# Optimization experiments

Measured on AMD Instinct MI355X. Metric: run time of the kernel, lower is better.

The kernel has to match this reference:

```python
import jax, jax.numpy as jnp
import numpy as np

N, D, H, C = 50000, 128, 4, 16  # nodes, in_dim, heads, out per head
E, ED = 800000, 64              # edges, edge feature dim
NEG_SLOPE = 0.2


def setup_inputs() -> dict:
    key = jax.random.key(0)
    ks = jax.random.split(key, 10)
    x = jax.random.normal(ks[0], (N, D), dtype=jnp.float32)
    edge_index = jax.random.randint(ks[1], (2, E), 0, N, dtype=jnp.int64)
    edge_attr = jax.random.normal(ks[2], (E, ED), dtype=jnp.float32)
    s = 0.1
    W = jax.random.normal(ks[3], (H * C, D), dtype=jnp.float32) * s       # lin (no bias)
    W_edge = jax.random.normal(ks[4], (H * C, ED), dtype=jnp.float32) * s  # lin_edge (no bias)
    att_src = jax.random.normal(ks[5], (H, C), dtype=jnp.float32) * s
    att_dst = jax.random.normal(ks[6], (H, C), dtype=jnp.float32) * s
    att_edge = jax.random.normal(ks[7], (H, C), dtype=jnp.float32) * s
    bias = jnp.zeros((H * C,), dtype=jnp.float32)
    return dict(x=x, edge_index=edge_index, edge_attr=edge_attr, W=W,
                W_edge=W_edge, att_src=att_src, att_dst=att_dst,
                att_edge=att_edge, bias=bias)


def reference(x, edge_index, edge_attr, W, W_edge, att_src, att_dst, att_edge, bias):
    n = x.shape[0]
    src0, dst0 = edge_index[0], edge_index[1]

    # PyG GATConv default: add self-loops, self-loop edge_attr = per-dst mean of incoming edge_attr
    ones = jnp.ones((src0.shape[0],), dtype=edge_attr.dtype)
    cnt = jax.ops.segment_sum(ones, dst0, num_segments=n)                # [N]
    loop_attr = jax.ops.segment_sum(edge_attr, dst0, num_segments=n)
    loop_attr = loop_attr / jnp.maximum(cnt, 1.0)[:, None]               # [N, ED]
    ar = jnp.arange(n, dtype=src0.dtype)
    src = jnp.concatenate([src0, ar])
    dst = jnp.concatenate([dst0, ar])
    ea = jnp.concatenate([edge_attr, loop_attr], axis=0)                 # [E+N, ED]

    xh = (x @ W.T).reshape(n, H, C)                                      # [N, H, C]
    a_src = jnp.einsum('nhc,hc->nh', xh, att_src)                        # [N, H]
    a_dst = jnp.einsum('nhc,hc->nh', xh, att_dst)
    eh = (ea @ W_edge.T).reshape(-1, H, C)                               # [E+N, H, C]
    a_edge = jnp.einsum('ehc,hc->eh', eh, att_edge)                      # [E+N, H]

    alpha = a_src[src] + a_dst[dst] + a_edge                             # [E+N, H]
    alpha = jax.nn.leaky_relu(alpha, NEG_SLOPE)

    # softmax over edges grouped by destination node (PyG softmax)
    amax = jax.ops.segment_max(alpha, dst, num_segments=n)               # [N, H]
    alpha = jnp.exp(alpha - amax[dst])
    denom = jax.ops.segment_sum(alpha, dst, num_segments=n)
    alpha = alpha / (denom[dst] + 1e-16)

    # message = x_j * alpha, scatter-add to destination
    out = jax.ops.segment_sum(xh[src] * alpha[:, :, None], dst, num_segments=n)  # [N,H,C]
    return out.reshape(n, H * C) + bias
```

## Files before the change

### kernel.cpp

```cpp
#include <hip/hip_runtime.h>
#include <math.h>

#define N_NODES 50000
#define DIM     128
#define NHEAD   4
#define NCH     16
#define HC      64
#define NE      800000
#define EDIM    64
#define NEG     0.2f

__device__ __forceinline__ float lrelu(float v) { return v > 0.f ? v : NEG * v; }

__global__ void k1_vedge(const float* __restrict__ W_edge, const float* __restrict__ att_edge,
                         float* __restrict__ v_edge) {
    int t = threadIdx.x;
    int h = t >> 6, d = t & 63;
    float acc = 0.f;
    #pragma unroll
    for (int c = 0; c < NCH; ++c)
        acc = fmaf(att_edge[h * NCH + c], W_edge[(h * NCH + c) * EDIM + d], acc);
    v_edge[h * 64 + d] = acc;
}

__global__ __launch_bounds__(256) void k2_xh(const float* __restrict__ x, const float* __restrict__ W,
                                             const float* __restrict__ att_src, const float* __restrict__ att_dst,
                                             float* __restrict__ xh, float* __restrict__ a_src,
                                             float* __restrict__ a_dst) {
    __shared__ float Wt[128 * 68];
    int t = threadIdx.x;
    for (int idx = t; idx < 64 * 128; idx += 256) {
        int col = idx >> 7, k = idx & 127;
        Wt[k * 68 + col] = W[idx];
    }
    __syncthreads();

    int h  = t & 3;
    int rp = t >> 2;
    int row0 = blockIdx.x * 128 + rp * 2;
    int r0 = min(row0, N_NODES - 1);
    int r1 = min(row0 + 1, N_NODES - 1);
    const float4* x0 = (const float4*)(x + (size_t)r0 * DIM);
    const float4* x1 = (const float4*)(x + (size_t)r1 * DIM);

    float acc0[16], acc1[16];
    #pragma unroll
    for (int c = 0; c < 16; ++c) { acc0[c] = 0.f; acc1[c] = 0.f; }

    for (int k4 = 0; k4 < 32; ++k4) {
        float4 xa = x0[k4];
        float4 xb = x1[k4];
        #pragma unroll
        for (int kk = 0; kk < 4; ++kk) {
            float va = (&xa.x)[kk];
            float vb = (&xb.x)[kk];
            const float* wr = &Wt[(k4 * 4 + kk) * 68 + h * 16];
            #pragma unroll
            for (int j = 0; j < 4; ++j) {
                float4 w = *(const float4*)(wr + 4 * j);
                acc0[4 * j + 0] = fmaf(va, w.x, acc0[4 * j + 0]);
                acc0[4 * j + 1] = fmaf(va, w.y, acc0[4 * j + 1]);
                acc0[4 * j + 2] = fmaf(va, w.z, acc0[4 * j + 2]);
                acc0[4 * j + 3] = fmaf(va, w.w, acc0[4 * j + 3]);
                acc1[4 * j + 0] = fmaf(vb, w.x, acc1[4 * j + 0]);
                acc1[4 * j + 1] = fmaf(vb, w.y, acc1[4 * j + 1]);
                acc1[4 * j + 2] = fmaf(vb, w.z, acc1[4 * j + 2]);
                acc1[4 * j + 3] = fmaf(vb, w.w, acc1[4 * j + 3]);
            }
        }
    }

    if (row0 < N_NODES) {
        float4* o = (float4*)(xh + (size_t)row0 * HC + h * 16);
        o[0] = make_float4(acc0[0], acc0[1], acc0[2], acc0[3]);
        o[1] = make_float4(acc0[4], acc0[5], acc0[6], acc0[7]);
        o[2] = make_float4(acc0[8], acc0[9], acc0[10], acc0[11]);
        o[3] = make_float4(acc0[12], acc0[13], acc0[14], acc0[15]);
        float ss = 0.f, sd = 0.f;
        #pragma unroll
        for (int c = 0; c < 16; ++c) {
            ss = fmaf(acc0[c], att_src[h * 16 + c], ss);
            sd = fmaf(acc0[c], att_dst[h * 16 + c], sd);
        }
        a_src[row0 * 4 + h] = ss;
        a_dst[row0 * 4 + h] = sd;
    }
    if (row0 + 1 < N_NODES) {
        float4* o = (float4*)(xh + (size_t)(row0 + 1) * HC + h * 16);
        o[0] = make_float4(acc1[0], acc1[1], acc1[2], acc1[3]);
        o[1] = make_float4(acc1[4], acc1[5], acc1[6], acc1[7]);
        o[2] = make_float4(acc1[8], acc1[9], acc1[10], acc1[11]);
        o[3] = make_float4(acc1[12], acc1[13], acc1[14], acc1[15]);
        float ss = 0.f, sd = 0.f;
        #pragma unroll
        for (int c = 0; c < 16; ++c) {
            ss = fmaf(acc1[c], att_src[h * 16 + c], ss);
            sd = fmaf(acc1[c], att_dst[h * 16 + c], sd);
        }
        a_src[(row0 + 1) * 4 + h] = ss;
        a_dst[(row0 + 1) * 4 + h] = sd;
    }
}

__global__ __launch_bounds__(256) void ka_deg(const int* __restrict__ ei, int* __restrict__ deg) {
    int e = blockIdx.x * 256 + threadIdx.x;
    if (e >= NE) return;
    atomicAdd(deg + ei[NE + e], 1);
}

__global__ void k4a_scan(const int* __restrict__ deg, int* __restrict__ tmp, int* __restrict__ bsums) {
    int t = threadIdx.x;
    int i = blockIdx.x * 256 + t;
    int v = (i < N_NODES) ? deg[i] : 0;
    int lane = t & 63, w = t >> 6;
    int xv = v;
    #pragma unroll
    for (int o = 1; o < 64; o <<= 1) {
        int y = __shfl_up(xv, o);
        if (lane >= o) xv += y;
    }
    __shared__ int wtot[4];
    if (lane == 63) wtot[w] = xv;
    __syncthreads();
    int add = 0;
    #pragma unroll
    for (int j = 0; j < 4; ++j)
        if (j < w) add += wtot[j];
    xv += add;
    if (i < N_NODES) tmp[i] = xv;
    if (t == 255) bsums[blockIdx.x] = xv;
}

__global__ void k4b_scan(int* __restrict__ bsums, int nb) {
    int t = threadIdx.x;
    int v = (t < nb) ? bsums[t] : 0;
    int lane = t & 63, w = t >> 6;
    int xv = v;
    #pragma unroll
    for (int o = 1; o < 64; o <<= 1) {
        int y = __shfl_up(xv, o);
        if (lane >= o) xv += y;
    }
    __shared__ int wtot[4];
    if (lane == 63) wtot[w] = xv;
    __syncthreads();
    int add = 0;
    #pragma unroll
    for (int j = 0; j < 4; ++j)
        if (j < w) add += wtot[j];
    xv += add;
    if (t < nb) bsums[t] = xv - v;
}

__global__ void k4c_finish(const int* __restrict__ tmp, const int* __restrict__ bsums,
                           const int* __restrict__ deg, int* __restrict__ rowptr,
                           int* __restrict__ cursor) {
    int i = blockIdx.x * 256 + threadIdx.x;
    if (i >= N_NODES) return;
    int incl = tmp[i] + bsums[i >> 8];
    rowptr[i + 1] = incl;
    cursor[i] = incl - deg[i];
    if (i == 0) rowptr[0] = 0;
}

__global__ __launch_bounds__(256) void kb_edge(const float* __restrict__ edge_attr,
                                               const int* __restrict__ ei,
                                               const float* __restrict__ v_edge,
                                               int* __restrict__ cursor,
                                               int* __restrict__ csr_src,
                                               float* __restrict__ csr_p) {
    __shared__ float4 sv[64];
    int t = threadIdx.x;
    if (t < 64) sv[t] = ((const float4*)v_edge)[t];
    __syncthreads();
    int e = blockIdx.x * 256 + t;
    if (e >= NE) return;

    const float4* ea = (const float4*)(edge_attr + (size_t)e * EDIM);
    float p0 = 0.f, p1 = 0.f, p2 = 0.f, p3 = 0.f;
    #pragma unroll
    for (int j = 0; j < 16; ++j) {
        float4 v  = ea[j];
        float4 w0 = sv[j], w1 = sv[16 + j], w2 = sv[32 + j], w3 = sv[48 + j];
        p0 = fmaf(v.x, w0.x, fmaf(v.y, w0.y, fmaf(v.z, w0.z, fmaf(v.w, w0.w, p0))));
        p1 = fmaf(v.x, w1.x, fmaf(v.y, w1.y, fmaf(v.z, w1.z, fmaf(v.w, w1.w, p1))));
        p2 = fmaf(v.x, w2.x, fmaf(v.y, w2.y, fmaf(v.z, w2.z, fmaf(v.w, w2.w, p2))));
        p3 = fmaf(v.x, w3.x, fmaf(v.y, w3.y, fmaf(v.z, w3.z, fmaf(v.w, w3.w, p3))));
    }
    int src = ei[e];
    int dst = ei[NE + e];
    int pos = atomicAdd(cursor + dst, 1);
    csr_src[pos] = src;
    *(float4*)(csr_p + (size_t)pos * 4) = make_float4(p0, p1, p2, p3);
}

__global__ __launch_bounds__(256) void k6_agg(const int* __restrict__ rowptr,
                                              const int* __restrict__ csr_src,
                                              const float* __restrict__ csr_p,
                                              const float* __restrict__ xh,
                                              const float* __restrict__ a_src,
                                              const float* __restrict__ a_dst,
                                              const float* __restrict__ bias,
                                              float* __restrict__ out) {
    int lane = threadIdx.x & 63;
    int n = blockIdx.x * 4 + (threadIdx.x >> 6);
    if (n >= N_NODES) return;
    int start = rowptr[n], end = rowptr[n + 1];
    int degn = end - start;

    int h = lane & 3;
    float adh = a_dst[n * 4 + h];
    float sw = 0.f, sp = 0.f;
    for (int i = start + (lane >> 2); i < end; i += 16) {
        int s  = csr_src[i];
        float p = csr_p[(size_t)i * 4 + h];
        float a = a_src[(size_t)s * 4 + h];
        sw += __expf(lrelu(a + adh + p));
        sp += p;
    }
    sw += __shfl_xor(sw, 4);  sp += __shfl_xor(sp, 4);
    sw += __shfl_xor(sw, 8);  sp += __shfl_xor(sp, 8);
    sw += __shfl_xor(sw, 16); sp += __shfl_xor(sp, 16);
    sw += __shfl_xor(sw, 32); sp += __shfl_xor(sp, 32);

    float al    = sp / fmaxf((float)degn, 1.f);
    float wself = __expf(lrelu(a_src[n * 4 + h] + adh + al));
    float denom = sw + wself + 1e-16f;

    int h2 = lane >> 4;
    float d2   = __shfl(denom, h2);
    float ws2  = __shfl(wself, h2);
    float adh2 = __shfl(adh, h2);
    float acc = ws2 * xh[(size_t)n * HC + lane];

    int i = start;
    for (; i + 4 <= end; i += 4) {
        int s0 = csr_src[i], s1 = csr_src[i + 1], s2 = csr_src[i + 2], s3 = csr_src[i + 3];
        float p0 = csr_p[(size_t)(i + 0) * 4 + h2];
        float p1 = csr_p[(size_t)(i + 1) * 4 + h2];
        float p2 = csr_p[(size_t)(i + 2) * 4 + h2];
        float p3 = csr_p[(size_t)(i + 3) * 4 + h2];
        float w0 = __expf(lrelu(a_src[(size_t)s0 * 4 + h2] + adh2 + p0));
        float w1 = __expf(lrelu(a_src[(size_t)s1 * 4 + h2] + adh2 + p1));
        float w2 = __expf(lrelu(a_src[(size_t)s2 * 4 + h2] + adh2 + p2));
        float w3 = __expf(lrelu(a_src[(size_t)s3 * 4 + h2] + adh2 + p3));
        float x0 = xh[(size_t)s0 * HC + lane];
        float x1 = xh[(size_t)s1 * HC + lane];
        float x2 = xh[(size_t)s2 * HC + lane];
        float x3 = xh[(size_t)s3 * HC + lane];
        acc = fmaf(w0, x0, acc);
        acc = fmaf(w1, x1, acc);
        acc = fmaf(w2, x2, acc);
        acc = fmaf(w3, x3, acc);
    }
    for (; i < end; ++i) {
        int sv = csr_src[i];
        float pv = csr_p[(size_t)i * 4 + h2];
        float wv = __expf(lrelu(a_src[(size_t)sv * 4 + h2] + adh2 + pv));
        acc = fmaf(wv, xh[(size_t)sv * HC + lane], acc);
    }
    out[(size_t)n * HC + lane] = acc / d2 + bias[lane];
}

extern "C" void kernel_launch(void* const* d_in, const int* in_sizes, int n_in,
                              void* d_out, int out_size, void* d_ws, size_t ws_size,
                              hipStream_t stream) {
    const float* x         = (const float*)d_in[0];
    const int*   ei        = (const int*)d_in[1];
    const float* edge_attr = (const float*)d_in[2];
    const float* W         = (const float*)d_in[3];
    const float* W_edge    = (const float*)d_in[4];
    const float* att_src   = (const float*)d_in[5];
    const float* att_dst   = (const float*)d_in[6];
    const float* att_edge  = (const float*)d_in[7];
    const float* bias      = (const float*)d_in[8];
    float* out = (float*)d_out;

    char* ws = (char*)d_ws;
    size_t off = 0;
    float* v_edge    = (float*)(ws + off); off += 1024;
    float* xh        = (float*)(ws + off); off += (size_t)N_NODES * HC * 4;
    float* a_src     = (float*)(ws + off); off += (size_t)N_NODES * 4 * 4;
    float* a_dst     = (float*)(ws + off); off += (size_t)N_NODES * 4 * 4;
    int*   deg       = (int*)(ws + off);   off += (size_t)N_NODES * 4;
    int*   tmp       = (int*)(ws + off);   off += (size_t)N_NODES * 4;
    int*   bsums     = (int*)(ws + off);   off += 1024;
    int*   rowptr    = (int*)(ws + off);   off += (size_t)(N_NODES + 4) * 4;
    int*   cursor    = (int*)(ws + off);   off += (size_t)N_NODES * 4;
    int*   csr_src   = (int*)(ws + off);   off += (size_t)NE * 4;
    float* csr_p     = (float*)(ws + off); off += (size_t)NE * 4 * 4;

    hipMemsetAsync(deg, 0, (size_t)N_NODES * 4, stream);

    k1_vedge<<<1, 256, 0, stream>>>(W_edge, att_edge, v_edge);
    k2_xh<<<(N_NODES + 127) / 128, 256, 0, stream>>>(x, W, att_src, att_dst, xh, a_src, a_dst);
    ka_deg<<<(NE + 255) / 256, 256, 0, stream>>>(ei, deg);
    int nb = (N_NODES + 255) / 256;
    k4a_scan<<<nb, 256, 0, stream>>>(deg, tmp, bsums);
    k4b_scan<<<1, 256, 0, stream>>>(bsums, nb);
    k4c_finish<<<nb, 256, 0, stream>>>(tmp, bsums, deg, rowptr, cursor);
    kb_edge<<<(NE + 255) / 256, 256, 0, stream>>>(edge_attr, ei, v_edge, cursor, csr_src, csr_p);
    k6_agg<<<(N_NODES + 3) / 4, 256, 0, stream>>>(rowptr, csr_src, csr_p, xh,
                                                  a_src, a_dst, bias, out);
}
```

Measured before the change: 468.6 us.

## Compute edge projections coalesced in edge order and build CSR as permutation

```diff
diff --git a/kernel.cpp b/kernel.cpp
--- a/kernel.cpp
+++ b/kernel.cpp
@@ -102,10 +102,41 @@
     }
 }
 
-__global__ __launch_bounds__(256) void ka_deg(const int* __restrict__ ei, int* __restrict__ deg) {
-    int e = blockIdx.x * 256 + threadIdx.x;
-    if (e >= NE) return;
-    atomicAdd(deg + ei[NE + e], 1);
+__global__ __launch_bounds__(256) void kp_edge(const float* __restrict__ edge_attr,
+                                               const int* __restrict__ ei,
+                                               const float* __restrict__ v_edge,
+                                               float* __restrict__ p_e,
+                                               int* __restrict__ deg) {
+    int lane = threadIdx.x & 63;
+    int q = lane & 15;
+    float4 w0 = *(const float4*)(v_edge + 0 * 64 + q * 4);
+    float4 w1 = *(const float4*)(v_edge + 1 * 64 + q * 4);
+    float4 w2 = *(const float4*)(v_edge + 2 * 64 + q * 4);
+    float4 w3 = *(const float4*)(v_edge + 3 * 64 + q * 4);
+
+    int wave   = (blockIdx.x * 256 + threadIdx.x) >> 6;
+    int nwaves = gridDim.x * 4;
+    for (int g = wave; g < NE / 4; g += nwaves) {
+        float4 v = *(const float4*)(edge_attr + (size_t)g * 256 + lane * 4);
+        float p0 = fmaf(v.x, w0.x, fmaf(v.y, w0.y, fmaf(v.z, w0.z, v.w * w0.w)));
+        float p1 = fmaf(v.x, w1.x, fmaf(v.y, w1.y, fmaf(v.z, w1.z, v.w * w1.w)));
+        float p2 = fmaf(v.x, w2.x, fmaf(v.y, w2.y, fmaf(v.z, w2.z, v.w * w2.w)));
+        float p3 = fmaf(v.x, w3.x, fmaf(v.y, w3.y, fmaf(v.z, w3.z, v.w * w3.w)));
+        #pragma unroll
+        for (int m = 1; m < 16; m <<= 1) {
+            p0 += __shfl_xor(p0, m);
+            p1 += __shfl_xor(p1, m);
+            p2 += __shfl_xor(p2, m);
+            p3 += __shfl_xor(p3, m);
+        }
+        int e = g * 4 + (lane >> 4);
+        if (q < 4) {
+            float pv = (q == 0) ? p0 : (q == 1) ? p1 : (q == 2) ? p2 : p3;
+            p_e[(size_t)e * 4 + q] = pv;
+        }
+        if (q == 0)
+            atomicAdd(deg + ei[NE + e], 1);
+    }
 }
 
 __global__ void k4a_scan(const int* __restrict__ deg, int* __restrict__ tmp, int* __restrict__ bsums) {
@@ -163,40 +194,20 @@
     if (i == 0) rowptr[0] = 0;
 }
 
-__global__ __launch_bounds__(256) void kb_edge(const float* __restrict__ edge_attr,
-                                               const int* __restrict__ ei,
-                                               const float* __restrict__ v_edge,
+__global__ __launch_bounds__(256) void k5_perm(const int* __restrict__ ei,
                                                int* __restrict__ cursor,
-                                               int* __restrict__ csr_src,
-                                               float* __restrict__ csr_p) {
-    __shared__ float4 sv[64];
-    int t = threadIdx.x;
-    if (t < 64) sv[t] = ((const float4*)v_edge)[t];
-    __syncthreads();
-    int e = blockIdx.x * 256 + t;
+                                               int* __restrict__ perm) {
+    int e = blockIdx.x * 256 + threadIdx.x;
     if (e >= NE) return;
-
-    const float4* ea = (const float4*)(edge_attr + (size_t)e * EDIM);
-    float p0 = 0.f, p1 = 0.f, p2 = 0.f, p3 = 0.f;
-    #pragma unroll
-    for (int j = 0; j < 16; ++j) {
-        float4 v  = ea[j];
-        float4 w0 = sv[j], w1 = sv[16 + j], w2 = sv[32 + j], w3 = sv[48 + j];
-        p0 = fmaf(v.x, w0.x, fmaf(v.y, w0.y, fmaf(v.z, w0.z, fmaf(v.w, w0.w, p0))));
-        p1 = fmaf(v.x, w1.x, fmaf(v.y, w1.y, fmaf(v.z, w1.z, fmaf(v.w, w1.w, p1))));
-        p2 = fmaf(v.x, w2.x, fmaf(v.y, w2.y, fmaf(v.z, w2.z, fmaf(v.w, w2.w, p2))));
-        p3 = fmaf(v.x, w3.x, fmaf(v.y, w3.y, fmaf(v.z, w3.z, fmaf(v.w, w3.w, p3))));
-    }
-    int src = ei[e];
     int dst = ei[NE + e];
     int pos = atomicAdd(cursor + dst, 1);
-    csr_src[pos] = src;
-    *(float4*)(csr_p + (size_t)pos * 4) = make_float4(p0, p1, p2, p3);
+    perm[pos] = e;
 }
 
 __global__ __launch_bounds__(256) void k6_agg(const int* __restrict__ rowptr,
-                                              const int* __restrict__ csr_src,
-                                              const float* __restrict__ csr_p,
+                                              const int* __restrict__ perm,
+                                              const int* __restrict__ ei,
+                                              const float* __restrict__ p_e,
                                               const float* __restrict__ xh,
                                               const float* __restrict__ a_src,
                                               const float* __restrict__ a_dst,
@@ -212,8 +223,9 @@
     float adh = a_dst[n * 4 + h];
     float sw = 0.f, sp = 0.f;
     for (int i = start + (lane >> 2); i < end; i += 16) {
-        int s  = csr_src[i];
-        float p = csr_p[(size_t)i * 4 + h];
+        int e  = perm[i];
+        int s  = ei[e];
+        float p = p_e[(size_t)e * 4 + h];
         float a = a_src[(size_t)s * 4 + h];
         sw += __expf(lrelu(a + adh + p));
         sp += p;
@@ -235,11 +247,12 @@
 
     int i = start;
     for (; i + 4 <= end; i += 4) {
-        int s0 = csr_src[i], s1 = csr_src[i + 1], s2 = csr_src[i + 2], s3 = csr_src[i + 3];
-        float p0 = csr_p[(size_t)(i + 0) * 4 + h2];
-        float p1 = csr_p[(size_t)(i + 1) * 4 + h2];
-        float p2 = csr_p[(size_t)(i + 2) * 4 + h2];
-        float p3 = csr_p[(size_t)(i + 3) * 4 + h2];
+        int e0 = perm[i], e1 = perm[i + 1], e2 = perm[i + 2], e3 = perm[i + 3];
+        int s0 = ei[e0], s1 = ei[e1], s2 = ei[e2], s3 = ei[e3];
+        float p0 = p_e[(size_t)e0 * 4 + h2];
+        float p1 = p_e[(size_t)e1 * 4 + h2];
+        float p2 = p_e[(size_t)e2 * 4 + h2];
+        float p3 = p_e[(size_t)e3 * 4 + h2];
         float w0 = __expf(lrelu(a_src[(size_t)s0 * 4 + h2] + adh2 + p0));
         float w1 = __expf(lrelu(a_src[(size_t)s1 * 4 + h2] + adh2 + p1));
         float w2 = __expf(lrelu(a_src[(size_t)s2 * 4 + h2] + adh2 + p2));
@@ -254,8 +267,9 @@
         acc = fmaf(w3, x3, acc);
     }
     for (; i < end; ++i) {
-        int sv = csr_src[i];
-        float pv = csr_p[(size_t)i * 4 + h2];
+        int ev = perm[i];
+        int sv = ei[ev];
+        float pv = p_e[(size_t)ev * 4 + h2];
         float wv = __expf(lrelu(a_src[(size_t)sv * 4 + h2] + adh2 + pv));
         acc = fmaf(wv, xh[(size_t)sv * HC + lane], acc);
     }
@@ -287,19 +301,19 @@
     int*   bsums     = (int*)(ws + off);   off += 1024;
     int*   rowptr    = (int*)(ws + off);   off += (size_t)(N_NODES + 4) * 4;
     int*   cursor    = (int*)(ws + off);   off += (size_t)N_NODES * 4;
-    int*   csr_src   = (int*)(ws + off);   off += (size_t)NE * 4;
-    float* csr_p     = (float*)(ws + off); off += (size_t)NE * 4 * 4;
+    int*   perm      = (int*)(ws + off);   off += (size_t)NE * 4;
+    float* p_e       = (float*)(ws + off); off += (size_t)NE * 4 * 4;
 
     hipMemsetAsync(deg, 0, (size_t)N_NODES * 4, stream);
 
     k1_vedge<<<1, 256, 0, stream>>>(W_edge, att_edge, v_edge);
     k2_xh<<<(N_NODES + 127) / 128, 256, 0, stream>>>(x, W, att_src, att_dst, xh, a_src, a_dst);
-    ka_deg<<<(NE + 255) / 256, 256, 0, stream>>>(ei, deg);
+    kp_edge<<<1024, 256, 0, stream>>>(edge_attr, ei, v_edge, p_e, deg);
     int nb = (N_NODES + 255) / 256;
     k4a_scan<<<nb, 256, 0, stream>>>(deg, tmp, bsums);
     k4b_scan<<<1, 256, 0, stream>>>(bsums, nb);
     k4c_finish<<<nb, 256, 0, stream>>>(tmp, bsums, deg, rowptr, cursor);
-    kb_edge<<<(NE + 255) / 256, 256, 0, stream>>>(edge_attr, ei, v_edge, cursor, csr_src, csr_p);
-    k6_agg<<<(N_NODES + 3) / 4, 256, 0, stream>>>(rowptr, csr_src, csr_p, xh,
+    k5_perm<<<(NE + 255) / 256, 256, 0, stream>>>(ei, cursor, perm);
+    k6_agg<<<(N_NODES + 3) / 4, 256, 0, stream>>>(rowptr, perm, ei, p_e, xh,
                                                   a_src, a_dst, bias, out);
 }
```

New measurement: 492.7 us. +5.2%, slower.
